# Performance work log

Measured on AMD Instinct MI355X. Metric: run time of the kernel, lower is better.

Reference implementation:

```python
import jax, jax.numpy as jnp
import numpy as np

# dims
B, C, H, W = 8, 256, 64, 128
P = 4                      # patch size (p1 == p2)
E = C // 2                 # embed dim = ngf//2 = Mamba d_model
HP, WP = H // P, W // P
N = HP * WP                # 512 tokens
DM = E                     # Mamba d_model
DI = 2 * DM                # d_inner (expand=2)
DS = 16                    # d_state
DC = 4                     # d_conv
DR = DM // 16              # dt_rank
NG = 128                   # new_ngf
S = 2                      # pixel-shuffle stride


def setup_inputs() -> dict:
    key = jax.random.key(0)
    ks = jax.random.split(key, 16)
    g = lambda i, shape, s=0.02: jax.random.normal(ks[i], shape, jnp.float32) * s
    return {
        'x': jax.random.normal(ks[0], (B, C, H, W), jnp.float32),
        # patch embed (conv k=stride=P)
        'patch_w': g(1, (E, C, P, P)),
        'patch_b': jnp.zeros((E,), jnp.float32),
        # Mamba params
        'in_proj_w': g(2, (2 * DI, DM)),
        'conv1d_w': g(3, (DI, DC), 0.1),
        'conv1d_b': jnp.zeros((DI,), jnp.float32),
        'x_proj_w': g(4, (DR + 2 * DS, DI)),
        'dt_proj_w': g(5, (DI, DR), 0.1),
        'dt_proj_b': jnp.full((DI,), -3.0, jnp.float32),
        'A_log': jnp.log(jnp.broadcast_to(jnp.arange(1, DS + 1, dtype=jnp.float32), (DI, DS))),
        'D_param': jnp.ones((DI,), jnp.float32),
        'out_proj_w': g(6, (DM, DI)),
        # unpatchify linear N -> N*P*P
        'lin_w': g(7, (N * P * P, N)),
        'lin_b': jnp.zeros((N * P * P,), jnp.float32),
        # nerv conv (3x3, out = new_ngf*S*S)
        'conv_w': g(8, (NG * S * S, E, 3, 3), 0.05),
        'conv_b': jnp.zeros((NG * S * S,), jnp.float32),
        # residual FFN (1x1)
        'ffn_w1': g(9, (NG, NG)),
        'ffn_b1': jnp.zeros((NG,), jnp.float32),
        'ffn_w2': g(10, (NG, NG)),
        'ffn_b2': jnp.zeros((NG,), jnp.float32),
    }


def reference(x, patch_w, patch_b, in_proj_w, conv1d_w, conv1d_b, x_proj_w,
              dt_proj_w, dt_proj_b, A_log, D_param, out_proj_w, lin_w, lin_b,
              conv_w, conv_b, ffn_w1, ffn_b1, ffn_w2, ffn_b2):
    silu = jax.nn.silu
    # ---- patch embed: (B,C,H,W) -> (B,N,E)
    t = jax.lax.conv_general_dilated(x, patch_w, (P, P), 'VALID',
                                     dimension_numbers=('NCHW', 'OIHW', 'NCHW'))
    t = t + patch_b[None, :, None, None]
    t = t.reshape(B, E, N).transpose(0, 2, 1)  # (B,N,E)

    # ---- Mamba selective scan
    xz = jnp.einsum('bld,ed->ble', t, in_proj_w)      # (B,N,2*DI)
    xin, z = jnp.split(xz, 2, axis=-1)
    # depthwise causal conv1d over sequence
    xp = jnp.pad(xin, ((0, 0), (DC - 1, 0), (0, 0)))
    xc = sum(xp[:, k:k + N, :] * conv1d_w[:, k] for k in range(DC)) + conv1d_b
    xc = silu(xc)                                     # (B,N,DI)
    dbl = jnp.einsum('bld,ed->ble', xc, x_proj_w)
    dt, Bs, Cs = dbl[..., :DR], dbl[..., DR:DR + DS], dbl[..., DR + DS:]
    dt = jax.nn.softplus(jnp.einsum('blr,dr->bld', dt, dt_proj_w) + dt_proj_b)
    A = -jnp.exp(A_log)                               # (DI,DS)
    dA = jnp.exp(dt[..., None] * A)                   # (B,N,DI,DS)
    dBx = dt[..., None] * Bs[:, :, None, :] * xc[..., None]

    def step(h, inputs):
        dA_t, dBx_t, C_t = inputs
        h = dA_t * h + dBx_t                          # (B,DI,DS)
        y = jnp.einsum('bdn,bn->bd', h, C_t)
        return h, y

    h0 = jnp.zeros((B, DI, DS), xc.dtype)
    _, ys = jax.lax.scan(step, h0, (dA.transpose(1, 0, 2, 3),
                                    dBx.transpose(1, 0, 2, 3),
                                    Cs.transpose(1, 0, 2)))
    y = ys.transpose(1, 0, 2) + D_param * xc
    y = y * silu(z)
    out = jnp.einsum('bld,ed->ble', y, out_proj_w)    # (B,N,DM)

    # ---- unpatchify: (B,N,E) -> (B,E,H,W)
    u = out.transpose(0, 2, 1)                        # (B,E,N)
    u = jnp.einsum('ben,mn->bem', u, lin_w) + lin_b   # (B,E,N*P*P)
    u = u.reshape(B, E, HP, WP, P, P).transpose(0, 1, 2, 4, 3, 5)
    u = u.reshape(B, E, H, W)

    # ---- nerv block: 3x3 conv -> pixel shuffle -> gelu
    c = jax.lax.conv_general_dilated(u, conv_w, (1, 1), ((1, 1), (1, 1)),
                                     dimension_numbers=('NCHW', 'OIHW', 'NCHW'))
    c = c + conv_b[None, :, None, None]               # (B,NG*S*S,H,W)
    c = c.reshape(B, NG, S, S, H, W).transpose(0, 1, 4, 2, 5, 3)
    c = c.reshape(B, NG, H * S, W * S)
    c = jax.nn.gelu(c)

    # ---- residual FFN (1x1 convs over channels)
    f = jax.nn.gelu(jnp.einsum('bchw,ec->behw', c, ffn_w1) + ffn_b1[None, :, None, None])
    f = jnp.einsum('behw,ce->bchw', f, ffn_w2) + ffn_b2[None, :, None, None]
    return c + f
```

## Files before the change

kernel.cpp:

```cpp
#include <hip/hip_runtime.h>
#include <hip/hip_bf16.h>

#define HW2 32768

typedef __attribute__((ext_vector_type(8))) short short8v;
typedef __attribute__((ext_vector_type(4))) float f32x4;

__device__ __forceinline__ float siluf(float x){ return x / (1.f + __expf(-x)); }
__device__ __forceinline__ float geluf(float v){
  float t = 0.7978845608028654f * fmaf(0.044715f*v*v, v, v);
  t = fminf(fmaxf(t, -15.f), 15.f);
  float e = __expf(2.f*t);
  return 0.5f*v*(1.f + (e-1.f)/(e+1.f));
}
__device__ __forceinline__ ushort bf16rne(float f){
  unsigned u = __float_as_uint(f);
  unsigned r = (u + 0x7fffu + ((u >> 16) & 1u)) >> 16;
  return (ushort)r;
}
__device__ __forceinline__ float bf2f(ushort u){ return __uint_as_float(((unsigned)u) << 16); }
__device__ __forceinline__ void split2(float v, ushort& h, ushort& lo){
  h = bf16rne(v);
  lo = bf16rne(v - bf2f(h));
}

__global__ __launch_bounds__(256) void k_zb(uint4* __restrict__ ubf4){
  int bid = blockIdx.x;
  int tid = threadIdx.x;
  uint4 z = make_uint4(0,0,0,0);
  size_t base4 = (size_t)bid * 34320;
  for (int i = tid; i < 1552; i += 256) {
    size_t off;
    if (i < 520)       off = i;
    else if (i < 1040) off = 33800 + (i - 520);
    else {
      int j = i - 1040;
      int row = 1 + (j >> 3);
      int colsel = (j >> 2) & 1, q = j & 3;
      off = (size_t)row*520 + colsel*516 + q;
    }
    ubf4[base4 + off] = z;
  }
}

__global__ __launch_bounds__(256) void k_wprep(const float* __restrict__ cw, ushort* __restrict__ wbf){
  int idx = blockIdx.x*256 + threadIdx.x;
  int j    = idx & 7;
  int lane = (idx >> 3) & 63;
  int f    = (idx >> 9) & 3;
  int tap  = (idx >> 11) % 9;
  int rest = idx / 18432;
  int ec = rest & 3, ocg = rest >> 2;
  int o = ocg*64 + f*16 + (lane & 15);
  int e = ec*32 + (lane >> 4)*8 + j;
  float v = cw[((size_t)o*128 + e)*9 + tap];
  wbf[idx] = bf16rne(v);
}

__global__ __launch_bounds__(256) void k_wffn(const float* __restrict__ w1, const float* __restrict__ w2,
                                              ushort* __restrict__ wpad){
  int idx = blockIdx.x*256 + threadIdx.x;
  int which = idx / 17408;
  int rem = idx - which*17408;
  int e = rem / 136, k = rem - e*136;
  const float* s = which ? w2 : w1;
  wpad[idx] = (k < 128) ? bf16rne(s[e*128 + k]) : (ushort)0;
}

__global__ __launch_bounds__(256) void k_wlin(const float* __restrict__ lw, ushort* __restrict__ lwbf){
  int i = blockIdx.x*256 + threadIdx.x;
  float4 v = reinterpret_cast<const float4*>(lw)[i];
  uint2 u;
  u.x = (uint)bf16rne(v.x) | ((uint)bf16rne(v.y) << 16);
  u.y = (uint)bf16rne(v.z) | ((uint)bf16rne(v.w) << 16);
  reinterpret_cast<uint2*>(lwbf)[i] = u;
}

__global__ __launch_bounds__(256) void k_ytr(const float* __restrict__ yo, ushort* __restrict__ ybfT){
  __shared__ float tile[32][132];
  int b = blockIdx.x, n0 = blockIdx.y*32;
  int tid = threadIdx.x;
  for (int it = 0; it < 16; ++it) {
    int idx = it*256 + tid;
    int row = idx >> 7, e = idx & 127;
    tile[row][e] = yo[((size_t)(b*512 + n0 + row))*128 + e];
  }
  __syncthreads();
  int e = tid >> 1, half = tid & 1;
  uint* dst = reinterpret_cast<uint*>(ybfT + ((size_t)b*128 + e)*512 + n0 + half*16);
  #pragma unroll
  for (int j = 0; j < 8; ++j) {
    int n = half*16 + j*2;
    dst[j] = (uint)bf16rne(tile[n][e]) | ((uint)bf16rne(tile[n+1][e]) << 16);
  }
}

__global__ __launch_bounds__(256) void k_patchm(const float* __restrict__ x, const float* __restrict__ pw,
                                                float* __restrict__ part){
  __shared__ ushort Ah[4096], Al[4096], Wh[4096], Wl[4096];
  int m0 = blockIdx.x * 128;
  int ks = blockIdx.y;
  int tid = threadIdx.x;
  int l = tid & 63, wv = tid >> 6;
  int wm = wv >> 1, we = wv & 1;
  int lj = l & 15, lg = l >> 4;
  f32x4 acc[4][4];
  #pragma unroll
  for (int a = 0; a < 4; ++a)
    #pragma unroll
    for (int b = 0; b < 4; ++b)
      acc[a][b] = (f32x4){0.f,0.f,0.f,0.f};
  int kbase = ks * 512;

  for (int it = 0; it < 16; ++it) {
    int k0 = kbase + it*32;
    __syncthreads();
    #pragma unroll
    for (int q = 0; q < 4; ++q) {
      int flat = q*256 + tid;
      int row = flat & 127, kk4 = flat >> 7;
      int m = m0 + row;
      int bb = m >> 9, ll = m & 511;
      int hp = ll >> 5, wp = ll & 31;
      int k = k0 + kk4*4;
      int c = k >> 4, i2 = (k >> 2) & 3;
      float4 v = *reinterpret_cast<const float4*>(x + (((bb*256 + c)*64 + hp*4 + i2)*128 + wp*4));
      ushort h0,h1,h2,h3,q0,q1,q2,q3;
      split2(v.x,h0,q0); split2(v.y,h1,q1); split2(v.z,h2,q2); split2(v.w,h3,q3);
      uint2 uh, ul;
      uh.x = (uint)h0 | ((uint)h1 << 16); uh.y = (uint)h2 | ((uint)h3 << 16);
      ul.x = (uint)q0 | ((uint)q1 << 16); ul.y = (uint)q2 | ((uint)q3 << 16);
      int lane = ((kk4 >> 1) << 4) | (row & 15);
      int dst = ((row >> 4)*64 + lane)*8 + (kk4 & 1)*4;
      *reinterpret_cast<uint2*>(Ah + dst) = uh;
      *reinterpret_cast<uint2*>(Al + dst) = ul;
    }
    #pragma unroll
    for (int q = 0; q < 4; ++q) {
      int flat = q*256 + tid;
      int e = flat >> 3, kk4 = flat & 7;
      float4 v = *reinterpret_cast<const float4*>(pw + (size_t)e*4096 + k0 + kk4*4);
      ushort h0,h1,h2,h3,q0,q1,q2,q3;
      split2(v.x,h0,q0); split2(v.y,h1,q1); split2(v.z,h2,q2); split2(v.w,h3,q3);
      uint2 uh, ul;
      uh.x = (uint)h0 | ((uint)h1 << 16); uh.y = (uint)h2 | ((uint)h3 << 16);
      ul.x = (uint)q0 | ((uint)q1 << 16); ul.y = (uint)q2 | ((uint)q3 << 16);
      int lane = ((kk4 >> 1) << 4) | (e & 15);
      int dst = ((e >> 4)*64 + lane)*8 + (kk4 & 1)*4;
      *reinterpret_cast<uint2*>(Wh + dst) = uh;
      *reinterpret_cast<uint2*>(Wl + dst) = ul;
    }
    __syncthreads();

    short8v ah[4], al_[4], wh[4], wl_[4];
    #pragma unroll
    for (int f = 0; f < 4; ++f) {
      ah[f]  = *reinterpret_cast<const short8v*>(Ah + ((wm*4 + f)*64 + l)*8);
      al_[f] = *reinterpret_cast<const short8v*>(Al + ((wm*4 + f)*64 + l)*8);
      wh[f]  = *reinterpret_cast<const short8v*>(Wh + ((we*4 + f)*64 + l)*8);
      wl_[f] = *reinterpret_cast<const short8v*>(Wl + ((we*4 + f)*64 + l)*8);
    }
    #pragma unroll
    for (int fo = 0; fo < 4; ++fo)
      #pragma unroll
      for (int fj = 0; fj < 4; ++fj) {
        acc[fo][fj] = __builtin_amdgcn_mfma_f32_16x16x32_bf16(ah[fo],  wh[fj],  acc[fo][fj], 0, 0, 0);
        acc[fo][fj] = __builtin_amdgcn_mfma_f32_16x16x32_bf16(ah[fo],  wl_[fj], acc[fo][fj], 0, 0, 0);
        acc[fo][fj] = __builtin_amdgcn_mfma_f32_16x16x32_bf16(al_[fo], wh[fj],  acc[fo][fj], 0, 0, 0);
      }
  }
  float* pb = part + (size_t)ks*524288;
  #pragma unroll
  for (int fo = 0; fo < 4; ++fo) {
    int m = m0 + wm*64 + fo*16 + lg*4;
    #pragma unroll
    for (int fj = 0; fj < 4; ++fj) {
      int e = we*64 + fj*16 + lj;
      f32x4 a = acc[fo][fj];
      pb[(size_t)(m+0)*128 + e] = a.x;
      pb[(size_t)(m+1)*128 + e] = a.y;
      pb[(size_t)(m+2)*128 + e] = a.z;
      pb[(size_t)(m+3)*128 + e] = a.w;
    }
  }
}

__global__ __launch_bounds__(256) void k_tred(const float* __restrict__ part, const float* __restrict__ pb,
                                              float* __restrict__ t){
  int i = blockIdx.x*256 + threadIdx.x;
  const float4* p4 = reinterpret_cast<const float4*>(part);
  float4 s = reinterpret_cast<const float4*>(pb)[i & 31];
  #pragma unroll
  for (int ks = 0; ks < 8; ++ks) {
    float4 v = p4[(size_t)ks*131072 + i];
    s.x += v.x; s.y += v.y; s.z += v.z; s.w += v.w;
  }
  reinterpret_cast<float4*>(t)[i] = s;
}

__global__ __launch_bounds__(256) void k_gemm(const float* __restrict__ A, const float* __restrict__ W,
                                              float* __restrict__ C, int M, int N, int K){
  __shared__ __align__(16) float As[16][68];
  __shared__ __align__(16) float Bs[16][68];
  int m0 = blockIdx.x * 64, n0 = blockIdx.y * 64;
  int tid = threadIdx.x;
  int tm = tid >> 4, tn = tid & 15;
  int lm = tid >> 2, kq = tid & 3;
  float acc[4][4] = {};
  const float* Abase = A + (size_t)(m0 + lm)*K + kq*4;
  const float* Wbase = W + (size_t)(n0 + lm)*K + kq*4;
  for (int k0 = 0; k0 < K; k0 += 16) {
    float4 av = *reinterpret_cast<const float4*>(Abase + k0);
    float4 bv = *reinterpret_cast<const float4*>(Wbase + k0);
    As[kq*4+0][lm]=av.x; As[kq*4+1][lm]=av.y; As[kq*4+2][lm]=av.z; As[kq*4+3][lm]=av.w;
    Bs[kq*4+0][lm]=bv.x; Bs[kq*4+1][lm]=bv.y; Bs[kq*4+2][lm]=bv.z; Bs[kq*4+3][lm]=bv.w;
    __syncthreads();
    #pragma unroll
    for (int kk = 0; kk < 16; ++kk) {
      float4 a = *reinterpret_cast<const float4*>(&As[kk][tm*4]);
      float4 b = *reinterpret_cast<const float4*>(&Bs[kk][tn*4]);
      float ar[4] = {a.x,a.y,a.z,a.w};
      float br[4] = {b.x,b.y,b.z,b.w};
      #pragma unroll
      for (int i = 0; i < 4; ++i)
        #pragma unroll
        for (int j = 0; j < 4; ++j)
          acc[i][j] = fmaf(ar[i], br[j], acc[i][j]);
    }
    __syncthreads();
  }
  #pragma unroll
  for (int i = 0; i < 4; ++i) {
    float4 ov = make_float4(acc[i][0], acc[i][1], acc[i][2], acc[i][3]);
    *reinterpret_cast<float4*>(C + (size_t)(m0 + tm*4 + i)*N + n0 + tn*4) = ov;
  }
}

__global__ __launch_bounds__(256) void k_conv1d(const float* __restrict__ xz, const float* __restrict__ w,
                                                const float* __restrict__ bias, float* __restrict__ xc){
  int idx = blockIdx.x*256 + threadIdx.x;
  int d = idx & 255;
  int l = (idx >> 8) & 511;
  int bb = idx >> 17;
  const float* base = xz + (size_t)bb*512*512 + d;
  float s = bias[d];
  #pragma unroll
  for (int k = 0; k < 4; ++k) {
    int ls = l - 3 + k;
    if (ls >= 0) s = fmaf(base[(size_t)ls*512], w[d*4+k], s);
  }
  xc[idx] = s / (1.f + __expf(-s));
}

__global__ __launch_bounds__(256) void k_xproj(const float* __restrict__ xc, const float* __restrict__ xpw,
                                               const float* __restrict__ dtw, const float* __restrict__ dtb,
                                               float* __restrict__ dbl, float* __restrict__ dt){
  __shared__ __align__(16) float sxc[256];
  __shared__ float sdbl[40];
  int bl = blockIdx.x;
  int tid = threadIdx.x;
  sxc[tid] = xc[(size_t)bl*256 + tid];
  __syncthreads();
  if (tid < 40) {
    const float4* wr = reinterpret_cast<const float4*>(xpw + tid*256);
    const float4* xr = reinterpret_cast<const float4*>(sxc);
    float s = 0.f;
    #pragma unroll 8
    for (int i = 0; i < 64; ++i) {
      float4 w = wr[i], xv = xr[i];
      s += w.x*xv.x + w.y*xv.y + w.z*xv.z + w.w*xv.w;
    }
    sdbl[tid] = s;
    dbl[(size_t)bl*40 + tid] = s;
  }
  __syncthreads();
  float s = dtb[tid];
  const float* wr = dtw + tid*8;
  #pragma unroll
  for (int r = 0; r < 8; ++r) s = fmaf(sdbl[r], wr[r], s);
  float sp = (s > 20.f) ? s : log1pf(__expf(s));
  dt[(size_t)bl*256 + tid] = sp;
}

__global__ __launch_bounds__(256) void k_scanA(const float* __restrict__ dt, const float* __restrict__ dbl,
                                               const float* __restrict__ xc, const float* __restrict__ A_log,
                                               float* __restrict__ aprod, float* __restrict__ hend){
  __shared__ float sdt[32][16], sxc[32][16], sB[32][16];
  int tid = threadIdx.x;
  int bg = blockIdx.x;
  int ch = blockIdx.y;
  int bb = bg >> 4, dgrp = bg & 15;
  int l0 = ch*32;
  #pragma unroll
  for (int it = 0; it < 2; ++it) {
    int idx = it*256 + tid;
    int t = idx >> 4, dd = idx & 15;
    int base = bb*512 + l0 + t;
    sdt[t][dd] = dt[(size_t)base*256 + dgrp*16 + dd];
    sxc[t][dd] = xc[(size_t)base*256 + dgrp*16 + dd];
    sB [t][dd] = dbl[(size_t)base*40 + 8 + dd];
  }
  __syncthreads();
  int n = tid & 15, dloc = tid >> 4;
  float Ac = -__expf(A_log[(dgrp*16 + dloc)*16 + n]);
  float a = 1.f, h = 0.f;
  #pragma unroll
  for (int t = 0; t < 32; ++t) {
    float dtv = sdt[t][dloc], xcv = sxc[t][dloc], Bv = sB[t][n];
    float dA = __expf(dtv*Ac);
    h = fmaf(dA, h, dtv*Bv*xcv);
    a *= dA;
  }
  aprod[(size_t)(bg*16 + ch)*256 + tid] = a;
  hend [(size_t)(bg*16 + ch)*256 + tid] = h;
}

__global__ __launch_bounds__(256) void k_scanB(const float* __restrict__ aprod, const float* __restrict__ hend,
                                               float* __restrict__ hstart){
  int tid = threadIdx.x;
  int bg = blockIdx.x;
  float hs = 0.f;
  #pragma unroll
  for (int ch = 0; ch < 16; ++ch) {
    size_t idx = (size_t)(bg*16 + ch)*256 + tid;
    hstart[idx] = hs;
    hs = fmaf(aprod[idx], hs, hend[idx]);
  }
}

__global__ __launch_bounds__(256) void k_scanC(const float* __restrict__ dt, const float* __restrict__ dbl,
                                               const float* __restrict__ xc, const float* __restrict__ xz,
                                               const float* __restrict__ A_log, const float* __restrict__ Dp,
                                               const float* __restrict__ hstart, float* __restrict__ y){
  __shared__ float sdt[32][16], sxc[32][16], sB[32][16], sC[32][16], sz[32][16];
  int tid = threadIdx.x;
  int bg = blockIdx.x;
  int ch = blockIdx.y;
  int bb = bg >> 4, dgrp = bg & 15;
  int l0 = ch*32;
  #pragma unroll
  for (int it = 0; it < 2; ++it) {
    int idx = it*256 + tid;
    int t = idx >> 4, dd = idx & 15;
    int base = bb*512 + l0 + t;
    sdt[t][dd] = dt[(size_t)base*256 + dgrp*16 + dd];
    sxc[t][dd] = xc[(size_t)base*256 + dgrp*16 + dd];
    sB [t][dd] = dbl[(size_t)base*40 + 8  + dd];
    sC [t][dd] = dbl[(size_t)base*40 + 24 + dd];
    sz [t][dd] = xz[(size_t)base*512 + 256 + dgrp*16 + dd];
  }
  __syncthreads();
  int n = tid & 15, dloc = tid >> 4;
  int d = dgrp*16 + dloc;
  float Ac = -__expf(A_log[d*16 + n]);
  float Dv = Dp[d];
  float h = hstart[(size_t)(bg*16 + ch)*256 + tid];
  #pragma unroll 4
  for (int t = 0; t < 32; ++t) {
    float dtv = sdt[t][dloc], xcv = sxc[t][dloc];
    float Bv = sB[t][n], Cv = sC[t][n];
    float dA = __expf(dtv*Ac);
    h = fmaf(dA, h, dtv*Bv*xcv);
    float yp = h*Cv;
    yp += __shfl_xor(yp, 1, 16);
    yp += __shfl_xor(yp, 2, 16);
    yp += __shfl_xor(yp, 4, 16);
    yp += __shfl_xor(yp, 8, 16);
    if (n == 0) {
      float zv = sz[t][dloc];
      y[(size_t)(bb*512 + l0 + t)*256 + d] = (yp + Dv*xcv) * (zv / (1.f + __expf(-zv)));
    }
  }
}

__global__ __launch_bounds__(512) void k_linm(const ushort* __restrict__ ybfT, const ushort* __restrict__ lwbf,
                                              const float* __restrict__ lb, ushort* __restrict__ ubf){
  __shared__ ushort As[128*88];
  __shared__ ushort Bs[128*88];
  int m0 = blockIdx.x * 128;
  int b  = blockIdx.y;
  int tid = threadIdx.x;
  int l = tid & 63, wv = tid >> 6;
  int wm = wv & 3, we = wv >> 2;
  int lj = l & 15, lg = l >> 4;
  f32x4 acc[4][2];
  #pragma unroll
  for (int fo = 0; fo < 4; ++fo)
    #pragma unroll
    for (int fj = 0; fj < 2; ++fj)
      acc[fo][fj] = (f32x4){0.f,0.f,0.f,0.f};

  for (int k0 = 0; k0 < 512; k0 += 64) {
    __syncthreads();
    #pragma unroll
    for (int it = 0; it < 2; ++it) {
      int flat = it*512 + tid;
      int e = flat >> 3, kc8 = flat & 7;
      *reinterpret_cast<uint4*>(&As[e*88 + kc8*8]) =
        *reinterpret_cast<const uint4*>(ybfT + ((size_t)b*128 + e)*512 + k0 + kc8*8);
      *reinterpret_cast<uint4*>(&Bs[e*88 + kc8*8]) =
        *reinterpret_cast<const uint4*>(lwbf + (size_t)(m0 + e)*512 + k0 + kc8*8);
    }
    __syncthreads();
    #pragma unroll
    for (int kc = 0; kc < 2; ++kc) {
      short8v af[4], bq[2];
      #pragma unroll
      for (int fo = 0; fo < 4; ++fo)
        af[fo] = *reinterpret_cast<const short8v*>(&As[(we*64 + fo*16 + lj)*88 + kc*32 + lg*8]);
      #pragma unroll
      for (int fj = 0; fj < 2; ++fj)
        bq[fj] = *reinterpret_cast<const short8v*>(&Bs[(wm*32 + fj*16 + lj)*88 + kc*32 + lg*8]);
      #pragma unroll
      for (int fo = 0; fo < 4; ++fo)
        #pragma unroll
        for (int fj = 0; fj < 2; ++fj)
          acc[fo][fj] = __builtin_amdgcn_mfma_f32_16x16x32_bf16(af[fo], bq[fj], acc[fo][fj], 0, 0, 0);
    }
  }
  #pragma unroll
  for (int fj = 0; fj < 2; ++fj) {
    int m = m0 + wm*32 + fj*16 + lj;
    float bias = lb[m];
    int hh = ((m >> 9) << 2) + ((m >> 2) & 3);
    int ww = (((m >> 4) & 31) << 2) + (m & 3);
    #pragma unroll
    for (int fo = 0; fo < 4; ++fo) {
      int eg = we*2 + (fo >> 1);
      int e5 = ((fo & 1) << 4) + (lg << 2);
      f32x4 a = acc[fo][fj];
      uint2 u;
      u.x = (uint)bf16rne(a.x + bias) | ((uint)bf16rne(a.y + bias) << 16);
      u.y = (uint)bf16rne(a.z + bias) | ((uint)bf16rne(a.w + bias) << 16);
      *reinterpret_cast<uint2*>(ubf + ((((size_t)b*4 + eg)*66 + hh + 1)*130 + ww + 1)*32 + e5) = u;
    }
  }
}

__global__ __launch_bounds__(256, 4) void k_conv3m(const ushort* __restrict__ ubf, const ushort* __restrict__ wbf,
                                                   const float* __restrict__ cb, ushort* __restrict__ cbf){
  __shared__ ushort wlds[18432];
  int h2 = blockIdx.x;
  int bz = blockIdx.y;
  int bb = bz >> 3, ocg = bz & 7;
  int tid = threadIdx.x;
  int l   = tid & 63;
  int wv  = tid >> 6;
  int hr  = wv >> 1;
  int wseg = (wv & 1) * 64;
  int lj = l & 15, lg = l >> 4;

  f32x4 acc[4][4];
  #pragma unroll
  for (int i = 0; i < 4; ++i)
    #pragma unroll
    for (int j = 0; j < 4; ++j)
      acc[i][j] = (f32x4){0.f, 0.f, 0.f, 0.f};

  for (int ec = 0; ec < 4; ++ec) {
    __syncthreads();
    const uint4* sA = reinterpret_cast<const uint4*>(wbf) + (size_t)(ocg*4 + ec)*2304;
    uint4* dA = reinterpret_cast<uint4*>(wlds);
    #pragma unroll
    for (int q = 0; q < 9; ++q) dA[q*256 + tid] = sA[q*256 + tid];
    __syncthreads();

    const ushort* ub_ec = ubf + (((size_t)(bb*4 + ec)*66 + 2*h2 + hr)*130 + wseg + lj)*32 + lg*8;
    #pragma unroll
    for (int ki = 0; ki < 3; ++ki) {
      const ushort* bbase_p = ub_ec + (size_t)ki*4160;
      #pragma unroll
      for (int kj = 0; kj < 3; ++kj) {
        const ushort* wtap = wlds + (ki*3 + kj)*2048 + l*8;
        short8v af[4], bfr[4];
        #pragma unroll
        for (int f = 0; f < 4; ++f)
          af[f] = *reinterpret_cast<const short8v*>(wtap + f*512);
        #pragma unroll
        for (int f = 0; f < 4; ++f)
          bfr[f] = *reinterpret_cast<const short8v*>(bbase_p + (f*16 + kj)*32);
        #pragma unroll
        for (int fo = 0; fo < 4; ++fo)
          #pragma unroll
          for (int fj = 0; fj < 4; ++fj)
            acc[fo][fj] = __builtin_amdgcn_mfma_f32_16x16x32_bf16(af[fo], bfr[fj], acc[fo][fj], 0, 0, 0);
      }
    }
  }

  int row = h2*2 + hr;
  #pragma unroll
  for (int fo = 0; fo < 4; ++fo) {
    int obase = ocg*64 + fo*16 + lg*4;
    int g = obase >> 2;
    float b0 = cb[obase], b1 = cb[obase+1], b2 = cb[obase+2], b3 = cb[obase+3];
    size_t rbase0 = (((size_t)bb*128 + g)*128 + 2*row)*256;
    size_t rbase1 = rbase0 + 256;
    #pragma unroll
    for (int fj = 0; fj < 4; ++fj) {
      int w = wseg + fj*16 + lj;
      f32x4 a = acc[fo][fj];
      uint u0 = (uint)bf16rne(geluf(a.x + b0)) | ((uint)bf16rne(geluf(a.y + b1)) << 16);
      uint u1 = (uint)bf16rne(geluf(a.z + b2)) | ((uint)bf16rne(geluf(a.w + b3)) << 16);
      *reinterpret_cast<uint*>(cbf + rbase0 + 2*w) = u0;
      *reinterpret_cast<uint*>(cbf + rbase1 + 2*w) = u1;
    }
  }
}

__global__ __launch_bounds__(512) void k_ffnm(const ushort* __restrict__ wpad, const float* __restrict__ b1,
                                              const float* __restrict__ b2, const ushort* __restrict__ cbf,
                                              float* __restrict__ out){
  extern __shared__ ushort sm[];
  ushort* cT = sm;
  ushort* wl = sm + 128*136;
  int pix0 = blockIdx.x * 128;
  int bb = pix0 >> 15;
  int hw0 = pix0 & 32767;
  int tid = threadIdx.x;
  int l = tid & 63, wv = tid >> 6;
  int wc = wv >> 2, wp = wv & 3;
  int lj = l & 15, lg = l >> 4;
  int r = tid & 1, hpair = tid >> 1;
  const ushort* cbase = cbf + (size_t)bb*128*HW2 + hw0;

  for (int it = 0; it < 16; ++it) {
    int flat = it*256 + hpair;
    int pp = flat & 63;
    int cpair = flat >> 6;
    int ch = cpair*2 + r;
    uint own = *reinterpret_cast<const uint*>(cbase + (size_t)ch*HW2 + pp*2);
    uint other = __shfl_xor((int)own, 1);
    uint o = r ? ((other >> 16) | (own & 0xffff0000u))
               : ((own & 0xffffu) | (other << 16));
    *reinterpret_cast<uint*>(&cT[(pp*2 + r)*136 + cpair*2]) = o;
  }
  {
    const uint4* src = reinterpret_cast<const uint4*>(wpad);
    uint4* dst = reinterpret_cast<uint4*>(wl);
    for (int i = tid; i < 2176; i += 512) dst[i] = src[i];
  }
  __syncthreads();

  f32x4 acc[4][2];
  #pragma unroll
  for (int fo = 0; fo < 4; ++fo)
    #pragma unroll
    for (int fj = 0; fj < 2; ++fj)
      acc[fo][fj] = (f32x4){0.f,0.f,0.f,0.f};

  #pragma unroll
  for (int kc = 0; kc < 4; ++kc) {
    short8v af[4], bq[2];
    #pragma unroll
    for (int fo = 0; fo < 4; ++fo)
      af[fo] = *reinterpret_cast<const short8v*>(&wl[(wc*64 + fo*16 + lj)*136 + kc*32 + lg*8]);
    #pragma unroll
    for (int fj = 0; fj < 2; ++fj)
      bq[fj] = *reinterpret_cast<const short8v*>(&cT[(wp*32 + fj*16 + lj)*136 + kc*32 + lg*8]);
    #pragma unroll
    for (int fo = 0; fo < 4; ++fo)
      #pragma unroll
      for (int fj = 0; fj < 2; ++fj)
        acc[fo][fj] = __builtin_amdgcn_mfma_f32_16x16x32_bf16(af[fo], bq[fj], acc[fo][fj], 0, 0, 0);
  }
  __syncthreads();

  const ushort* w2g = wpad + 17408;
  short8v a2[4], a2n[4];
  #pragma unroll
  for (int fo = 0; fo < 4; ++fo)
    a2[fo] = *reinterpret_cast<const short8v*>(w2g + (size_t)(wc*64 + fo*16 + lj)*136 + lg*8);

  #pragma unroll
  for (int fo = 0; fo < 4; ++fo) {
    int ch0 = wc*64 + fo*16 + lg*4;
    float c0 = b1[ch0], c1 = b1[ch0+1], c2 = b1[ch0+2], c3 = b1[ch0+3];
    #pragma unroll
    for (int fj = 0; fj < 2; ++fj) {
      int px = wp*32 + fj*16 + lj;
      f32x4 a = acc[fo][fj];
      uint2 u;
      u.x = (uint)bf16rne(geluf(a.x + c0)) | ((uint)bf16rne(geluf(a.y + c1)) << 16);
      u.y = (uint)bf16rne(geluf(a.z + c2)) | ((uint)bf16rne(geluf(a.w + c3)) << 16);
      *reinterpret_cast<uint2*>(&wl[px*136 + ch0]) = u;
    }
  }
  __syncthreads();

  #pragma unroll
  for (int fo = 0; fo < 4; ++fo)
    #pragma unroll
    for (int fj = 0; fj < 2; ++fj)
      acc[fo][fj] = (f32x4){0.f,0.f,0.f,0.f};

  #pragma unroll
  for (int kc = 0; kc < 4; ++kc) {
    if (kc < 3) {
      #pragma unroll
      for (int fo = 0; fo < 4; ++fo)
        a2n[fo] = *reinterpret_cast<const short8v*>(w2g + (size_t)(wc*64 + fo*16 + lj)*136 + (kc+1)*32 + lg*8);
    }
    short8v bq[2];
    #pragma unroll
    for (int fj = 0; fj < 2; ++fj)
      bq[fj] = *reinterpret_cast<const short8v*>(&wl[(wp*32 + fj*16 + lj)*136 + kc*32 + lg*8]);
    #pragma unroll
    for (int fo = 0; fo < 4; ++fo)
      #pragma unroll
      for (int fj = 0; fj < 2; ++fj)
        acc[fo][fj] = __builtin_amdgcn_mfma_f32_16x16x32_bf16(a2[fo], bq[fj], acc[fo][fj], 0, 0, 0);
    #pragma unroll
    for (int fo = 0; fo < 4; ++fo) a2[fo] = a2n[fo];
  }

  #pragma unroll
  for (int fo = 0; fo < 4; ++fo) {
    int ch0 = wc*64 + fo*16 + lg*4;
    float d0 = b2[ch0], d1 = b2[ch0+1], d2 = b2[ch0+2], d3 = b2[ch0+3];
    #pragma unroll
    for (int fj = 0; fj < 2; ++fj) {
      int px = wp*32 + fj*16 + lj;
      f32x4 a = acc[fo][fj];
      uint2 cu = *reinterpret_cast<const uint2*>(&cT[px*136 + ch0]);
      float cv0 = __uint_as_float((cu.x & 0xffffu) << 16);
      float cv1 = __uint_as_float(cu.x & 0xffff0000u);
      float cv2 = __uint_as_float((cu.y & 0xffffu) << 16);
      float cv3 = __uint_as_float(cu.y & 0xffff0000u);
      float* p0 = out + (size_t)bb*128*HW2 + (size_t)ch0*HW2 + hw0 + px;
      p0[0]             = cv0 + a.x + d0;
      p0[HW2]           = cv1 + a.y + d1;
      p0[2*HW2]         = cv2 + a.z + d2;
      p0[3*(size_t)HW2] = cv3 + a.w + d3;
    }
  }
}

extern "C" void kernel_launch(void* const* d_in, const int* in_sizes, int n_in,
                              void* d_out, int out_size, void* d_ws, size_t ws_size,
                              hipStream_t stream) {
  const float* x          = (const float*)d_in[0];
  const float* patch_w    = (const float*)d_in[1];
  const float* patch_b    = (const float*)d_in[2];
  const float* in_proj_w  = (const float*)d_in[3];
  const float* conv1d_w   = (const float*)d_in[4];
  const float* conv1d_b   = (const float*)d_in[5];
  const float* x_proj_w   = (const float*)d_in[6];
  const float* dt_proj_w  = (const float*)d_in[7];
  const float* dt_proj_b  = (const float*)d_in[8];
  const float* A_log      = (const float*)d_in[9];
  const float* D_param    = (const float*)d_in[10];
  const float* out_proj_w = (const float*)d_in[11];
  const float* lin_w      = (const float*)d_in[12];
  const float* lin_b      = (const float*)d_in[13];
  const float* conv_w     = (const float*)d_in[14];
  const float* conv_b     = (const float*)d_in[15];
  const float* ffn_w1     = (const float*)d_in[16];
  const float* ffn_b1     = (const float*)d_in[17];
  const float* ffn_w2     = (const float*)d_in[18];
  const float* ffn_b2     = (const float*)d_in[19];
  float* out = (float*)d_out;

  ushort* ubf  = (ushort*)d_ws;
  ushort* wbf  = ubf + 10982400;
  ushort* wpad = wbf + 589824;
  float* t    = (float*)(wpad + 34816);
  float* xz   = t    + 524288;
  float* xc   = xz   + 2097152;
  float* dbl  = xc   + 1048576;
  float* dt   = dbl  + 163840;
  float* y    = dt   + 1048576;
  float* yo   = y    + 1048576;
  float* apr  = yo   + 524288;
  float* hend = apr  + 524288;
  float* hst  = hend + 524288;
  ushort* lwbf = (ushort*)(hst + 524288);
  ushort* ybfT = lwbf + 4194304;
  ushort* cbf  = ybfT + 524288;
  float* part = xz;

  k_zb    <<<dim3(32), dim3(256), 0, stream>>>((uint4*)ubf);
  k_wprep <<<dim3(2304), dim3(256), 0, stream>>>(conv_w, wbf);
  k_wffn  <<<dim3(136), dim3(256), 0, stream>>>(ffn_w1, ffn_w2, wpad);
  k_wlin  <<<dim3(4096), dim3(256), 0, stream>>>(lin_w, lwbf);
  k_patchm<<<dim3(32, 8), dim3(256), 0, stream>>>(x, patch_w, part);
  k_tred  <<<dim3(512), dim3(256), 0, stream>>>(part, patch_b, t);
  k_gemm  <<<dim3(64, 8), dim3(256), 0, stream>>>(t, in_proj_w, xz, 4096, 512, 128);
  k_conv1d<<<dim3(4096), dim3(256), 0, stream>>>(xz, conv1d_w, conv1d_b, xc);
  k_xproj <<<dim3(4096), dim3(256), 0, stream>>>(xc, x_proj_w, dt_proj_w, dt_proj_b, dbl, dt);
  k_scanA <<<dim3(128, 16), dim3(256), 0, stream>>>(dt, dbl, xc, A_log, apr, hend);
  k_scanB <<<dim3(128), dim3(256), 0, stream>>>(apr, hend, hst);
  k_scanC <<<dim3(128, 16), dim3(256), 0, stream>>>(dt, dbl, xc, xz, A_log, D_param, hst, y);
  k_gemm  <<<dim3(64, 2), dim3(256), 0, stream>>>(y, out_proj_w, yo, 4096, 128, 256);
  k_ytr   <<<dim3(8, 16), dim3(256), 0, stream>>>(yo, ybfT);
  k_linm  <<<dim3(64, 8), dim3(512), 0, stream>>>(ybfT, lwbf, lin_b, ubf);
  k_conv3m<<<dim3(32, 64), dim3(256), 0, stream>>>(ubf, wbf, conv_b, cbf);
  k_ffnm  <<<dim3(2048), dim3(512), (size_t)(2*128*136)*sizeof(ushort), stream>>>(wpad, ffn_b1, ffn_b2, cbf, out);
}
```

Baseline: 358.8 us.

## Merge prep kernels, fold scan carry into scanC, retile conv3 and x_proj

Combines the four weight-prep and zeroing kernels into one launch, and removes k_scanB by having each scanC block recompute its chunk's starting state from the chunk products. It also doubles the split-K factor of the patch-embed GEMM for more blocks, and spreads the x_proj dot products over four lanes each with shuffle reduction. Separately, conv3m now uses 512-thread blocks covering two output-channel groups, so each B fragment is reused across 128 output channels at the cost of a larger LDS weight buffer. The scan recompute adds redundant serial work per block, and split-K doubles the partial-sum traffic.

After: 307.9 us. 1.17x faster.

```diff
diff --git a/kernel.cpp b/kernel.cpp
--- a/kernel.cpp
+++ b/kernel.cpp
@@ -24,56 +24,54 @@
   lo = bf16rne(v - bf2f(h));
 }
 
-__global__ __launch_bounds__(256) void k_zb(uint4* __restrict__ ubf4){
+__global__ __launch_bounds__(256) void k_prep(uint4* __restrict__ ubf4,
+                                              const float* __restrict__ cw, ushort* __restrict__ wbf,
+                                              const float* __restrict__ w1, const float* __restrict__ w2,
+                                              ushort* __restrict__ wpad,
+                                              const float* __restrict__ lw, ushort* __restrict__ lwbf){
   int bid = blockIdx.x;
   int tid = threadIdx.x;
-  uint4 z = make_uint4(0,0,0,0);
-  size_t base4 = (size_t)bid * 34320;
-  for (int i = tid; i < 1552; i += 256) {
-    size_t off;
-    if (i < 520)       off = i;
-    else if (i < 1040) off = 33800 + (i - 520);
-    else {
-      int j = i - 1040;
-      int row = 1 + (j >> 3);
-      int colsel = (j >> 2) & 1, q = j & 3;
-      off = (size_t)row*520 + colsel*516 + q;
-    }
-    ubf4[base4 + off] = z;
-  }
-}
-
-__global__ __launch_bounds__(256) void k_wprep(const float* __restrict__ cw, ushort* __restrict__ wbf){
-  int idx = blockIdx.x*256 + threadIdx.x;
-  int j    = idx & 7;
-  int lane = (idx >> 3) & 63;
-  int f    = (idx >> 9) & 3;
-  int tap  = (idx >> 11) % 9;
-  int rest = idx / 18432;
-  int ec = rest & 3, ocg = rest >> 2;
-  int o = ocg*64 + f*16 + (lane & 15);
-  int e = ec*32 + (lane >> 4)*8 + j;
-  float v = cw[((size_t)o*128 + e)*9 + tap];
-  wbf[idx] = bf16rne(v);
-}
-
-__global__ __launch_bounds__(256) void k_wffn(const float* __restrict__ w1, const float* __restrict__ w2,
-                                              ushort* __restrict__ wpad){
-  int idx = blockIdx.x*256 + threadIdx.x;
-  int which = idx / 17408;
-  int rem = idx - which*17408;
-  int e = rem / 136, k = rem - e*136;
-  const float* s = which ? w2 : w1;
-  wpad[idx] = (k < 128) ? bf16rne(s[e*128 + k]) : (ushort)0;
-}
-
-__global__ __launch_bounds__(256) void k_wlin(const float* __restrict__ lw, ushort* __restrict__ lwbf){
-  int i = blockIdx.x*256 + threadIdx.x;
-  float4 v = reinterpret_cast<const float4*>(lw)[i];
-  uint2 u;
-  u.x = (uint)bf16rne(v.x) | ((uint)bf16rne(v.y) << 16);
-  u.y = (uint)bf16rne(v.z) | ((uint)bf16rne(v.w) << 16);
-  reinterpret_cast<uint2*>(lwbf)[i] = u;
+  if (bid < 32) {
+    uint4 z = make_uint4(0,0,0,0);
+    size_t base4 = (size_t)bid * 34320;
+    for (int i = tid; i < 1552; i += 256) {
+      size_t off;
+      if (i < 520)       off = i;
+      else if (i < 1040) off = 33800 + (i - 520);
+      else {
+        int j = i - 1040;
+        int row = 1 + (j >> 3);
+        int colsel = (j >> 2) & 1, q = j & 3;
+        off = (size_t)row*520 + colsel*516 + q;
+      }
+      ubf4[base4 + off] = z;
+    }
+  } else if (bid < 2336) {
+    int idx = (bid - 32)*256 + tid;
+    int j    = idx & 7;
+    int lane = (idx >> 3) & 63;
+    int f    = (idx >> 9) & 3;
+    int tap  = (idx >> 11) % 9;
+    int rest = idx / 18432;
+    int ec = rest & 3, ocg = rest >> 2;
+    int o = ocg*64 + f*16 + (lane & 15);
+    int e = ec*32 + (lane >> 4)*8 + j;
+    wbf[idx] = bf16rne(cw[((size_t)o*128 + e)*9 + tap]);
+  } else if (bid < 2472) {
+    int idx = (bid - 2336)*256 + tid;
+    int which = idx / 17408;
+    int rem = idx - which*17408;
+    int e = rem / 136, k = rem - e*136;
+    const float* s = which ? w2 : w1;
+    wpad[idx] = (k < 128) ? bf16rne(s[e*128 + k]) : (ushort)0;
+  } else {
+    int i = (bid - 2472)*256 + tid;
+    float4 v = reinterpret_cast<const float4*>(lw)[i];
+    uint2 u;
+    u.x = (uint)bf16rne(v.x) | ((uint)bf16rne(v.y) << 16);
+    u.y = (uint)bf16rne(v.z) | ((uint)bf16rne(v.w) << 16);
+    reinterpret_cast<uint2*>(lwbf)[i] = u;
+  }
 }
 
 __global__ __launch_bounds__(256) void k_ytr(const float* __restrict__ yo, ushort* __restrict__ ybfT){
@@ -110,9 +108,9 @@
     #pragma unroll
     for (int b = 0; b < 4; ++b)
       acc[a][b] = (f32x4){0.f,0.f,0.f,0.f};
-  int kbase = ks * 512;
-
-  for (int it = 0; it < 16; ++it) {
+  int kbase = ks * 256;
+
+  for (int it = 0; it < 8; ++it) {
     int k0 = kbase + it*32;
     __syncthreads();
     #pragma unroll
@@ -191,7 +189,7 @@
   const float4* p4 = reinterpret_cast<const float4*>(part);
   float4 s = reinterpret_cast<const float4*>(pb)[i & 31];
   #pragma unroll
-  for (int ks = 0; ks < 8; ++ks) {
+  for (int ks = 0; ks < 16; ++ks) {
     float4 v = p4[(size_t)ks*131072 + i];
     s.x += v.x; s.y += v.y; s.z += v.z; s.w += v.w;
   }
@@ -261,17 +259,22 @@
   int tid = threadIdx.x;
   sxc[tid] = xc[(size_t)bl*256 + tid];
   __syncthreads();
-  if (tid < 40) {
-    const float4* wr = reinterpret_cast<const float4*>(xpw + tid*256);
-    const float4* xr = reinterpret_cast<const float4*>(sxc);
+  if (tid < 160) {
+    int g = tid >> 2, kq = tid & 3;
+    const float4* wr = reinterpret_cast<const float4*>(xpw + g*256) + kq;
+    const float4* xr = reinterpret_cast<const float4*>(sxc) + kq;
     float s = 0.f;
-    #pragma unroll 8
-    for (int i = 0; i < 64; ++i) {
-      float4 w = wr[i], xv = xr[i];
+    #pragma unroll
+    for (int i = 0; i < 16; ++i) {
+      float4 w = wr[i*4], xv = xr[i*4];
       s += w.x*xv.x + w.y*xv.y + w.z*xv.z + w.w*xv.w;
     }
-    sdbl[tid] = s;
-    dbl[(size_t)bl*40 + tid] = s;
+    s += __shfl_xor(s, 1);
+    s += __shfl_xor(s, 2);
+    if (kq == 0) {
+      sdbl[g] = s;
+      dbl[(size_t)bl*40 + g] = s;
+    }
   }
   __syncthreads();
   float s = dtb[tid];
@@ -315,23 +318,11 @@
   hend [(size_t)(bg*16 + ch)*256 + tid] = h;
 }
 
-__global__ __launch_bounds__(256) void k_scanB(const float* __restrict__ aprod, const float* __restrict__ hend,
-                                               float* __restrict__ hstart){
-  int tid = threadIdx.x;
-  int bg = blockIdx.x;
-  float hs = 0.f;
-  #pragma unroll
-  for (int ch = 0; ch < 16; ++ch) {
-    size_t idx = (size_t)(bg*16 + ch)*256 + tid;
-    hstart[idx] = hs;
-    hs = fmaf(aprod[idx], hs, hend[idx]);
-  }
-}
-
 __global__ __launch_bounds__(256) void k_scanC(const float* __restrict__ dt, const float* __restrict__ dbl,
                                                const float* __restrict__ xc, const float* __restrict__ xz,
                                                const float* __restrict__ A_log, const float* __restrict__ Dp,
-                                               const float* __restrict__ hstart, float* __restrict__ y){
+                                               const float* __restrict__ aprod, const float* __restrict__ hend,
+                                               float* __restrict__ y){
   __shared__ float sdt[32][16], sxc[32][16], sB[32][16], sC[32][16], sz[32][16];
   int tid = threadIdx.x;
   int bg = blockIdx.x;
@@ -349,12 +340,16 @@
     sC [t][dd] = dbl[(size_t)base*40 + 24 + dd];
     sz [t][dd] = xz[(size_t)base*512 + 256 + dgrp*16 + dd];
   }
+  float h = 0.f;
+  for (int cc = 0; cc < ch; ++cc) {
+    size_t idx = (size_t)(bg*16 + cc)*256 + tid;
+    h = fmaf(aprod[idx], h, hend[idx]);
+  }
   __syncthreads();
   int n = tid & 15, dloc = tid >> 4;
   int d = dgrp*16 + dloc;
   float Ac = -__expf(A_log[d*16 + n]);
   float Dv = Dp[d];
-  float h = hstart[(size_t)(bg*16 + ch)*256 + tid];
   #pragma unroll 4
   for (int t = 0; t < 32; ++t) {
     float dtv = sdt[t][dloc], xcv = sxc[t][dloc];
@@ -437,32 +432,32 @@
   }
 }
 
-__global__ __launch_bounds__(256, 4) void k_conv3m(const ushort* __restrict__ ubf, const ushort* __restrict__ wbf,
+__global__ __launch_bounds__(512, 4) void k_conv3m(const ushort* __restrict__ ubf, const ushort* __restrict__ wbf,
                                                    const float* __restrict__ cb, ushort* __restrict__ cbf){
-  __shared__ ushort wlds[18432];
+  __shared__ ushort wlds[36864];
   int h2 = blockIdx.x;
   int bz = blockIdx.y;
-  int bb = bz >> 3, ocg = bz & 7;
+  int bb = bz >> 2, op = bz & 3;
   int tid = threadIdx.x;
   int l   = tid & 63;
   int wv  = tid >> 6;
-  int hr  = wv >> 1;
-  int wseg = (wv & 1) * 64;
+  int hr  = wv >> 2;
+  int wseg = (wv & 3) * 32;
   int lj = l & 15, lg = l >> 4;
 
-  f32x4 acc[4][4];
-  #pragma unroll
-  for (int i = 0; i < 4; ++i)
-    #pragma unroll
-    for (int j = 0; j < 4; ++j)
+  f32x4 acc[8][2];
+  #pragma unroll
+  for (int i = 0; i < 8; ++i)
+    #pragma unroll
+    for (int j = 0; j < 2; ++j)
       acc[i][j] = (f32x4){0.f, 0.f, 0.f, 0.f};
 
   for (int ec = 0; ec < 4; ++ec) {
     __syncthreads();
-    const uint4* sA = reinterpret_cast<const uint4*>(wbf) + (size_t)(ocg*4 + ec)*2304;
+    const uint4* s0 = reinterpret_cast<const uint4*>(wbf) + (size_t)((op*2    )*4 + ec)*2304;
+    const uint4* s1 = reinterpret_cast<const uint4*>(wbf) + (size_t)((op*2 + 1)*4 + ec)*2304;
     uint4* dA = reinterpret_cast<uint4*>(wlds);
-    #pragma unroll
-    for (int q = 0; q < 9; ++q) dA[q*256 + tid] = sA[q*256 + tid];
+    for (int q = tid; q < 2304; q += 512) { dA[q] = s0[q]; dA[2304 + q] = s1[q]; }
     __syncthreads();
 
     const ushort* ub_ec = ubf + (((size_t)(bb*4 + ec)*66 + 2*h2 + hr)*130 + wseg + lj)*32 + lg*8;
@@ -471,33 +466,38 @@
       const ushort* bbase_p = ub_ec + (size_t)ki*4160;
       #pragma unroll
       for (int kj = 0; kj < 3; ++kj) {
-        const ushort* wtap = wlds + (ki*3 + kj)*2048 + l*8;
-        short8v af[4], bfr[4];
+        short8v bfr[2];
         #pragma unroll
-        for (int f = 0; f < 4; ++f)
-          af[f] = *reinterpret_cast<const short8v*>(wtap + f*512);
+        for (int f2 = 0; f2 < 2; ++f2)
+          bfr[f2] = *reinterpret_cast<const short8v*>(bbase_p + (f2*16 + kj)*32);
+        const ushort* wtap0 = wlds + (ki*3 + kj)*2048 + l*8;
         #pragma unroll
-        for (int f = 0; f < 4; ++f)
-          bfr[f] = *reinterpret_cast<const short8v*>(bbase_p + (f*16 + kj)*32);
-        #pragma unroll
-        for (int fo = 0; fo < 4; ++fo)
+        for (int half = 0; half < 2; ++half) {
+          const ushort* wtap = wtap0 + half*18432;
+          short8v af[4];
           #pragma unroll
-          for (int fj = 0; fj < 4; ++fj)
-            acc[fo][fj] = __builtin_amdgcn_mfma_f32_16x16x32_bf16(af[fo], bfr[fj], acc[fo][fj], 0, 0, 0);
+          for (int f = 0; f < 4; ++f)
+            af[f] = *reinterpret_cast<const short8v*>(wtap + f*512);
+          #pragma unroll
+          for (int fo = 0; fo < 4; ++fo)
+            #pragma unroll
+            for (int fj = 0; fj < 2; ++fj)
+              acc[half*4 + fo][fj] = __builtin_amdgcn_mfma_f32_16x16x32_bf16(af[fo], bfr[fj], acc[half*4 + fo][fj], 0, 0, 0);
+        }
       }
     }
   }
 
   int row = h2*2 + hr;
   #pragma unroll
-  for (int fo = 0; fo < 4; ++fo) {
-    int obase = ocg*64 + fo*16 + lg*4;
+  for (int fo = 0; fo < 8; ++fo) {
+    int obase = op*128 + fo*16 + lg*4;
     int g = obase >> 2;
     float b0 = cb[obase], b1 = cb[obase+1], b2 = cb[obase+2], b3 = cb[obase+3];
     size_t rbase0 = (((size_t)bb*128 + g)*128 + 2*row)*256;
     size_t rbase1 = rbase0 + 256;
     #pragma unroll
-    for (int fj = 0; fj < 4; ++fj) {
+    for (int fj = 0; fj < 2; ++fj) {
       int w = wseg + fj*16 + lj;
       f32x4 a = acc[fo][fj];
       uint u0 = (uint)bf16rne(geluf(a.x + b0)) | ((uint)bf16rne(geluf(a.y + b1)) << 16);
@@ -673,27 +673,22 @@
   float* yo   = y    + 1048576;
   float* apr  = yo   + 524288;
   float* hend = apr  + 524288;
-  float* hst  = hend + 524288;
-  ushort* lwbf = (ushort*)(hst + 524288);
+  ushort* lwbf = (ushort*)(hend + 524288);
   ushort* ybfT = lwbf + 4194304;
   ushort* cbf  = ybfT + 524288;
-  float* part = xz;
-
-  k_zb    <<<dim3(32), dim3(256), 0, stream>>>((uint4*)ubf);
-  k_wprep <<<dim3(2304), dim3(256), 0, stream>>>(conv_w, wbf);
-  k_wffn  <<<dim3(136), dim3(256), 0, stream>>>(ffn_w1, ffn_w2, wpad);
-  k_wlin  <<<dim3(4096), dim3(256), 0, stream>>>(lin_w, lwbf);
-  k_patchm<<<dim3(32, 8), dim3(256), 0, stream>>>(x, patch_w, part);
+  float* part = (float*)(cbf + 33554432);
+
+  k_prep  <<<dim3(6568), dim3(256), 0, stream>>>((uint4*)ubf, conv_w, wbf, ffn_w1, ffn_w2, wpad, lin_w, lwbf);
+  k_patchm<<<dim3(32, 16), dim3(256), 0, stream>>>(x, patch_w, part);
   k_tred  <<<dim3(512), dim3(256), 0, stream>>>(part, patch_b, t);
   k_gemm  <<<dim3(64, 8), dim3(256), 0, stream>>>(t, in_proj_w, xz, 4096, 512, 128);
   k_conv1d<<<dim3(4096), dim3(256), 0, stream>>>(xz, conv1d_w, conv1d_b, xc);
   k_xproj <<<dim3(4096), dim3(256), 0, stream>>>(xc, x_proj_w, dt_proj_w, dt_proj_b, dbl, dt);
   k_scanA <<<dim3(128, 16), dim3(256), 0, stream>>>(dt, dbl, xc, A_log, apr, hend);
-  k_scanB <<<dim3(128), dim3(256), 0, stream>>>(apr, hend, hst);
-  k_scanC <<<dim3(128, 16), dim3(256), 0, stream>>>(dt, dbl, xc, xz, A_log, D_param, hst, y);
+  k_scanC <<<dim3(128, 16), dim3(256), 0, stream>>>(dt, dbl, xc, xz, A_log, D_param, apr, hend, y);
   k_gemm  <<<dim3(64, 2), dim3(256), 0, stream>>>(y, out_proj_w, yo, 4096, 128, 256);
   k_ytr   <<<dim3(8, 16), dim3(256), 0, stream>>>(yo, ybfT);
   k_linm  <<<dim3(64, 8), dim3(512), 0, stream>>>(ybfT, lwbf, lin_b, ubf);
-  k_conv3m<<<dim3(32, 64), dim3(256), 0, stream>>>(ubf, wbf, conv_b, cbf);
+  k_conv3m<<<dim3(32, 32), dim3(512), 0, stream>>>(ubf, wbf, conv_b, cbf);
   k_ffnm  <<<dim3(2048), dim3(512), (size_t)(2*128*136)*sizeof(ushort), stream>>>(wpad, ffn_b1, ffn_b2, cbf, out);
 }
```
